# Performance work log

Measured on AMD Instinct MI355X. Metric: run time of the kernel, lower is better.

The kernel has to match this reference:

```python
import jax, jax.numpy as jnp
import numpy as np

CODEBOOK_SIZE = 4096
CODE_DIM = 256
N = 65536
COMMITMENT_COST = 0.25


def setup_inputs() -> dict:
    key = jax.random.key(0)
    k1, k2 = jax.random.split(key)
    z_flat = jax.random.normal(k1, (N, CODE_DIM), dtype=jnp.float32)
    # embedding initialized uniform(-1/codebook_size, 1/codebook_size) as in torch module
    emb_weight = jax.random.uniform(
        k2, (CODEBOOK_SIZE, CODE_DIM), dtype=jnp.float32,
        minval=-1.0 / CODEBOOK_SIZE, maxval=1.0 / CODEBOOK_SIZE)
    return {"z_flat": z_flat, "emb_weight": emb_weight}


def reference(z_flat, emb_weight):
    # squared L2 distances: [N, K] = |z|^2 + |e|^2 - 2 z e^T
    distances = (
        jnp.sum(z_flat ** 2, axis=1, keepdims=True)
        + jnp.sum(emb_weight ** 2, axis=1)
        - 2.0 * jnp.matmul(z_flat, emb_weight.T)
    )
    indices = jnp.argmin(distances, axis=1)  # [N]
    quantized = emb_weight[indices]          # [N, code_dim]

    e_latent_loss = jnp.mean((jax.lax.stop_gradient(quantized) - z_flat) ** 2)
    q_latent_loss = jnp.mean((quantized - jax.lax.stop_gradient(z_flat)) ** 2)
    loss = q_latent_loss + COMMITMENT_COST * e_latent_loss

    # straight-through estimator
    quantized_st = z_flat + jax.lax.stop_gradient(quantized - z_flat)
    return (loss, quantized_st, indices)
```

## Files before the change

kernel.cpp:

```cpp
#include <hip/hip_runtime.h>

#define KCODES 4096
#define DIM    256
#define NROWS  65536
#define MARGIN 4.0e-4f
#define DSLACK 3.0e-5f
#define LCAP   4096
#define CPAD   32
#define LSTRIDE (DIM + 4)

typedef unsigned long long u64;
typedef unsigned int  uint;
typedef unsigned short ushort;
typedef __attribute__((ext_vector_type(8))) short bf16x8;
typedef __attribute__((ext_vector_type(4))) float f32x4;

typedef __attribute__((address_space(3))) uint lds_u32_t;
typedef __attribute__((address_space(1))) uint glb_u32_t;

__device__ __forceinline__ void g2lds16(const void* g, void* l) {
    __builtin_amdgcn_global_load_lds((const glb_u32_t*)g, (lds_u32_t*)l, 16, 0, 0);
}

__device__ __forceinline__ float dppmin_quad(float m) {
    m = fminf(m, __int_as_float(__builtin_amdgcn_update_dpp(0, __float_as_int(m), 0xB1, 0xF, 0xF, true)));
    m = fminf(m, __int_as_float(__builtin_amdgcn_update_dpp(0, __float_as_int(m), 0x4E, 0xF, 0xF, true)));
    return m;
}
__device__ __forceinline__ float dppmin_row16(float m) {
    m = fminf(m, __int_as_float(__builtin_amdgcn_update_dpp(0, __float_as_int(m), 0x124, 0xF, 0xF, true)));
    m = fminf(m, __int_as_float(__builtin_amdgcn_update_dpp(0, __float_as_int(m), 0x128, 0xF, 0xF, true)));
    return m;
}
__device__ __forceinline__ uint dppor_row16(uint v) {
    v |= (uint)__builtin_amdgcn_update_dpp(0, (int)v, 0x124, 0xF, 0xF, true);
    v |= (uint)__builtin_amdgcn_update_dpp(0, (int)v, 0x128, 0xF, 0xF, true);
    return v;
}


__device__ __forceinline__ float np_half_sum128(const float4* __restrict__ p4) {
    #pragma clang fp contract(off)
    float4 v0 = p4[0], v1 = p4[1];
    float r0 = v0.x * v0.x, r1 = v0.y * v0.y, r2 = v0.z * v0.z, r3 = v0.w * v0.w;
    float r4 = v1.x * v1.x, r5 = v1.y * v1.y, r6 = v1.z * v1.z, r7 = v1.w * v1.w;
    #pragma unroll
    for (int i = 1; i < 16; ++i) {
        float4 a = p4[2 * i], b = p4[2 * i + 1];
        r0 += a.x * a.x; r1 += a.y * a.y; r2 += a.z * a.z; r3 += a.w * a.w;
        r4 += b.x * b.x; r5 += b.y * b.y; r6 += b.z * b.z; r7 += b.w * b.w;
    }
    return ((r0 + r1) + (r2 + r3)) + ((r4 + r5) + (r6 + r7));
}

__global__ void k_rownorm(const float* __restrict__ src, float* __restrict__ dst, int nrows) {
    int r = blockIdx.x * blockDim.x + threadIdx.x;
    if (r >= nrows) return;
    const float4* p4 = (const float4*)(src + (size_t)r * DIM);
    float s;
    {
        #pragma clang fp contract(off)
        s = np_half_sum128(p4) + np_half_sum128(p4 + 32);
    }
    dst[r] = s;
}

__device__ __forceinline__ float f32_dist(float Cr, float ebc, double accv) {
    #pragma clang fp contract(off)
    float A = Cr + ebc;
    float B = 2.0f * (float)accv;
    return A - B;
}

__device__ __forceinline__ ushort f2bf(float f) {
    uint u = __float_as_uint(f);
    return (ushort)((u + 0x7fffu + ((u >> 16) & 1u)) >> 16);
}


__global__ void k_split(const float* __restrict__ src, ushort* __restrict__ dst, int n8) {
    int i = blockIdx.x * blockDim.x + threadIdx.x;
    if (i >= n8) return;
    const float4* s4 = (const float4*)src;
    float4 a = s4[2 * i], b = s4[2 * i + 1];
    uint4 ov;
    ov.x = (uint)f2bf(a.x) | ((uint)f2bf(a.y) << 16);
    ov.y = (uint)f2bf(a.z) | ((uint)f2bf(a.w) << 16);
    ov.z = (uint)f2bf(b.x) | ((uint)f2bf(b.y) << 16);
    ov.w = (uint)f2bf(b.z) | ((uint)f2bf(b.w) << 16);
    *(uint4*)&dst[8 * i] = ov;
}

__global__ void k_init(int* __restrict__ cnt) {
    cnt[blockIdx.x * 256 + threadIdx.x] = 0;
}

__global__ __launch_bounds__(256, 2)
void k_gemm(const ushort* __restrict__ zh, const ushort* __restrict__ eh,
            const float* __restrict__ Crow, const float* __restrict__ eb2,
            float* __restrict__ tk, uint* __restrict__ tk2) {
    __shared__ __align__(16) ushort Bs[2][64 * 256];

    const int t = threadIdx.x;
    const int lane = t & 63;
    const int w = t >> 6;
    const int l15 = lane & 15, l4 = lane >> 4;
    const int row0w = blockIdx.x * 128 + w * 32;

    const char* ebp = (const char*)eh;

    auto stage = [&](int buf, int ct2) {
        const char* base = ebp + (size_t)ct2 * 64 * 512;
        #pragma unroll
        for (int i = 0; i < 8; ++i) {
            int idx = i * 256 + t;
            int code = idx >> 5;
            int c16  = idx & 31;
            int src  = (code << 9) + ((c16 ^ (code & 7)) << 4);
            g2lds16(base + src, (char*)Bs[buf] + idx * 16);
        }
    };

    bf16x8 a[2][8];
    #pragma unroll
    for (int f = 0; f < 2; ++f)
        #pragma unroll
        for (int ks = 0; ks < 8; ++ks)
            a[f][ks] = *(const bf16x8*)&zh[(size_t)(row0w + f * 16 + l15) * 256 + ks * 32 + l4 * 8];

    float crf[8];
    #pragma unroll
    for (int f = 0; f < 2; ++f)
        #pragma unroll
        for (int rg = 0; rg < 4; ++rg)
            crf[f * 4 + rg] = Crow[row0w + f * 16 + l4 * 4 + rg];

    float mprev[8];

    stage(0, 0);
    __syncthreads();

    #pragma unroll 2
    for (int ct2 = 0; ct2 < 64; ++ct2) {
        int buf = ct2 & 1;
        if (ct2 < 63) stage(buf ^ 1, ct2 + 1);

        f32x4 acc[2][4];
        #pragma unroll
        for (int f = 0; f < 2; ++f)
            #pragma unroll
            for (int cg = 0; cg < 4; ++cg) acc[f][cg] = (f32x4){0.f, 0.f, 0.f, 0.f};

        const ushort* Bb = Bs[buf];
        #pragma unroll
        for (int ks = 0; ks < 8; ++ks) {
            bf16x8 bfv[4];
            #pragma unroll
            for (int cg = 0; cg < 4; ++cg) {
                int rB = cg * 16 + l15;
                int off = rB * 256 + ((ks * 32 + l4 * 8) ^ ((l15 & 7) << 3));
                bfv[cg] = *(const bf16x8*)&Bb[off];
            }
            #pragma unroll
            for (int f = 0; f < 2; ++f)
                #pragma unroll
                for (int cg = 0; cg < 4; ++cg)
                    acc[f][cg] = __builtin_amdgcn_mfma_f32_16x16x32_bf16(
                        a[f][ks], bfv[cg], acc[f][cg], 0, 0, 0);
        }

        float ebv[4];
        #pragma unroll
        for (int cg = 0; cg < 4; ++cg) ebv[cg] = eb2[ct2 * 64 + cg * 16 + l15];

        #pragma unroll
        for (int f = 0; f < 2; ++f) {
            #pragma unroll
            for (int rg = 0; rg < 4; ++rg) {
                float m;
                {
                    #pragma clang fp contract(off)
                    m = 1e38f;
                    #pragma unroll
                    for (int cg = 0; cg < 4; ++cg) {
                        float A = crf[f * 4 + rg] + ebv[cg];
                        float d = A - 2.0f * acc[f][cg][rg];
                        m = fminf(m, d);
                    }
                }
                m = dppmin_quad(m);
                if ((ct2 & 1) == 0) {
                    mprev[f * 4 + rg] = m;
                } else {
                    m = fminf(m, mprev[f * 4 + rg]);
                    float mt = dppmin_row16(m);
                    int q = (int)((m - mt) * 1e5f);
                    q = q > 255 ? 255 : q;
                    uint pk = (uint)q << (8 * (l15 >> 2));
                    pk = dppor_row16(pk);
                    if (l15 == 0) {
                        int grow = row0w + f * 16 + l4 * 4 + rg;
                        int tt = ct2 >> 1;
                        tk [(size_t)tt * NROWS + grow] = mt;
                        tk2[(size_t)tt * NROWS + grow] = pk;
                    }
                }
            }
        }
        __syncthreads();
    }
}

__global__ void k_lists(const float* __restrict__ tk, const uint* __restrict__ tk2,
                        int* __restrict__ cnt, int* __restrict__ list,
                        u64* __restrict__ fkey) {
    int row = blockIdx.x * 256 + threadIdx.x;
    int lane = threadIdx.x & 63;
    float tm[32]; uint pk[32];
    #pragma unroll
    for (int tt = 0; tt < 32; ++tt) {
        tm[tt] = tk [(size_t)tt * NROWS + row];
        pk[tt] = tk2[(size_t)tt * NROWS + row];
    }
    float best = tm[0];
    #pragma unroll
    for (int tt = 1; tt < 32; ++tt) best = fminf(best, tm[tt]);
    fkey[row] = ~0ull;
    float cutoff = best + (MARGIN + DSLACK);

    #pragma unroll
    for (int tt = 0; tt < 32; ++tt) {
        #pragma unroll
        for (int p = 0; p < 4; ++p) {
            float v = tm[tt] + (float)((pk[tt] >> (8 * p)) & 255u) * 1e-5f;
            bool pred = v <= cutoff;
            u64 mask = __ballot(pred);
            if (mask) {
                int sub = tt * 4 + p;
                int nq = __popcll(mask);
                int rank = __popcll(mask & ((1ull << lane) - 1ull));
                int base = 0;
                if (lane == 0) base = atomicAdd(&cnt[sub * CPAD], nq);
                base = __shfl(base, 0, 64);
                int pos = base + rank;
                if (pred && pos < LCAP) list[sub * LCAP + pos] = row;
            }
        }
    }
}

__global__ __launch_bounds__(256, 2)
void k_exact(const float* __restrict__ z, const float* __restrict__ e,
             const float* __restrict__ Crow, const float* __restrict__ eb2,
             const int* __restrict__ list, const int* __restrict__ cnt,
             u64* __restrict__ fkey) {
    __shared__ __align__(16) float ex[32][260];
    __shared__ __align__(16) float zx[32][260];
    __shared__ int rows[32];
    __shared__ u64 keytab[32][17];
    const int sub = blockIdx.x;
    const int tile = sub >> 2, qq = sub & 3;
    const int nct = cnt[sub * CPAD];
    const int t = threadIdx.x;
    const int rp = t & 15, cs = t >> 4;

    {
        int cc = t >> 3, c8 = t & 7;
        int gcode = tile * 128 + (cc >> 2) * 16 + qq * 4 + (cc & 3);
        const float4* src = (const float4*)(e + (size_t)gcode * DIM);
        float4* dr = (float4*)ex[cc];
        #pragma unroll
        for (int j = 0; j < 8; ++j) dr[c8 + 8 * j] = src[c8 + 8 * j];
    }
    const int gc0 = tile * 128 + (cs >> 2) * 16 + qq * 4 + (cs & 3);
    const int gc1 = tile * 128 + ((cs >> 2) + 4) * 16 + qq * 4 + (cs & 3);
    const float ebc0 = eb2[gc0];
    const float ebc1 = eb2[gc1];

    for (int base = blockIdx.y * 32; base < nct; base += gridDim.y * 32) {
        __syncthreads();
        if (t < 32) {
            int i = base + t;
            rows[t] = list[sub * LCAP + (i < nct ? i : nct - 1)];
        }
        __syncthreads();
        {
            int rr = t >> 3, c8 = t & 7;
            const float4* src = (const float4*)(z + (size_t)rows[rr] * DIM);
            float4* dr = (float4*)zx[rr];
            #pragma unroll
            for (int j = 0; j < 8; ++j) dr[c8 + 8 * j] = src[c8 + 8 * j];
        }
        __syncthreads();

        double a00 = 0.0, a01 = 0.0, a10 = 0.0, a11 = 0.0;
        const float4* z0 = (const float4*)zx[rp];
        const float4* z1 = (const float4*)zx[rp + 16];
        const float4* e0 = (const float4*)ex[cs];
        const float4* e1 = (const float4*)ex[cs + 16];
        #pragma unroll 8
        for (int d4 = 0; d4 < 64; ++d4) {
            float4 x0 = z0[d4], x1 = z1[d4], y0 = e0[d4], y1 = e1[d4];
            a00 += (double)x0.x * (double)y0.x; a00 += (double)x0.y * (double)y0.y;
            a00 += (double)x0.z * (double)y0.z; a00 += (double)x0.w * (double)y0.w;
            a01 += (double)x0.x * (double)y1.x; a01 += (double)x0.y * (double)y1.y;
            a01 += (double)x0.z * (double)y1.z; a01 += (double)x0.w * (double)y1.w;
            a10 += (double)x1.x * (double)y0.x; a10 += (double)x1.y * (double)y0.y;
            a10 += (double)x1.z * (double)y0.z; a10 += (double)x1.w * (double)y0.w;
            a11 += (double)x1.x * (double)y1.x; a11 += (double)x1.y * (double)y1.y;
            a11 += (double)x1.z * (double)y1.z; a11 += (double)x1.w * (double)y1.w;
        }
        int r0 = rows[rp], r1 = rows[rp + 16];
        float C0 = Crow[r0], C1 = Crow[r1];
        u64 k00 = ((u64)__float_as_uint(f32_dist(C0, ebc0, a00)) << 32) | (u64)gc0;
        u64 k01 = ((u64)__float_as_uint(f32_dist(C0, ebc1, a01)) << 32) | (u64)gc1;
        u64 k10 = ((u64)__float_as_uint(f32_dist(C1, ebc0, a10)) << 32) | (u64)gc0;
        u64 k11 = ((u64)__float_as_uint(f32_dist(C1, ebc1, a11)) << 32) | (u64)gc1;
        keytab[rp][cs]      = k00 < k01 ? k00 : k01;
        keytab[rp + 16][cs] = k10 < k11 ? k10 : k11;
        __syncthreads();
        if (t < 32) {
            u64 kb = keytab[t][0];
            #pragma unroll
            for (int j = 1; j < 16; ++j) {
                u64 k = keytab[t][j];
                kb = k < kb ? k : kb;
            }
            atomicMin((unsigned long long*)&fkey[rows[t]], kb);
        }
    }
}

__global__ __launch_bounds__(256)
void k_gather(const float* __restrict__ z, const float* __restrict__ e,
              const u64* __restrict__ fkey, float* __restrict__ out,
              double* __restrict__ partial) {
    __shared__ double lred[4];
    const int t = threadIdx.x;
    const int row = blockIdx.x * 32 + (t >> 3);
    const int c8 = t & 7;
    const int idx = (int)(fkey[row] & 0xffffffffull);
    if (c8 == 0) out[1 + (size_t)NROWS * DIM + row] = (float)idx;
    const float4* zr = (const float4*)(z + (size_t)row * DIM);
    const float4* er = (const float4*)(e + (size_t)idx * DIM);
    float4* orow = (float4*)(out + 1 + (size_t)row * DIM);
    double lacc = 0.0;
    #pragma unroll
    for (int j = 0; j < 8; ++j) {
        float4 q = er[c8 + 8 * j];
        float4 zv = zr[c8 + 8 * j];
        orow[c8 + 8 * j] = q;
        double d0 = (double)q.x - (double)zv.x;
        double d1 = (double)q.y - (double)zv.y;
        double d2 = (double)q.z - (double)zv.z;
        double d3 = (double)q.w - (double)zv.w;
        lacc += d0 * d0 + d1 * d1 + d2 * d2 + d3 * d3;
    }
    for (int off = 32; off > 0; off >>= 1) lacc += __shfl_down(lacc, off, 64);
    if ((t & 63) == 0) lred[t >> 6] = lacc;
    __syncthreads();
    if (t == 0) partial[blockIdx.x] = lred[0] + lred[1] + lred[2] + lred[3];
}

__global__ void k_finish(const double* __restrict__ partial, float* __restrict__ out, int n) {
    __shared__ double s[256];
    double a = 0.0;
    for (int i = threadIdx.x; i < n; i += 256) a += partial[i];
    s[threadIdx.x] = a;
    __syncthreads();
    for (int off = 128; off > 0; off >>= 1) {
        if (threadIdx.x < off) s[threadIdx.x] += s[threadIdx.x + off];
        __syncthreads();
    }
    if (threadIdx.x == 0)
        out[0] = (float)(1.25 * s[0] / ((double)NROWS * (double)DIM));
}


__global__ __launch_bounds__(256, 1)
void k_main_slow(const float* __restrict__ z, const float* __restrict__ e,
                 const float* __restrict__ Crow, const float* __restrict__ eb2,
                 float* __restrict__ out, double* __restrict__ partial) {
    __shared__ float  zt[64][LSTRIDE];
    __shared__ float  et[64][LSTRIDE];
    __shared__ float  redd[64][17];
    __shared__ int    redi[64][17];
    __shared__ int    bsel[64];
    __shared__ double lred[4];

    const int t  = threadIdx.x;
    const int tx = t & 15;
    const int ty = t >> 4;
    const int row0 = blockIdx.x * 64;

    {
        const float4* zsrc = (const float4*)(z + (size_t)row0 * DIM);
        for (int i = t; i < 64 * (DIM / 4); i += 256) {
            int r = i >> 6, c4 = i & 63;
            *(float4*)&zt[r][c4 * 4] = zsrc[r * (DIM / 4) + c4];
        }
    }
    float Cr[4];
    #pragma unroll
    for (int ri = 0; ri < 4; ++ri) Cr[ri] = Crow[row0 + ty * 4 + ri];
    float bestd[4]; int besti[4];
    #pragma unroll
    for (int ri = 0; ri < 4; ++ri) { bestd[ri] = __int_as_float(0x7f800000); besti[ri] = 0; }

    for (int kt = 0; kt < KCODES / 64; ++kt) {
        __syncthreads();
        {
            const float4* esrc = (const float4*)(e + (size_t)kt * 64 * DIM);
            for (int i = t; i < 64 * (DIM / 4); i += 256) {
                int r = i >> 6, c4 = i & 63;
                *(float4*)&et[r][c4 * 4] = esrc[r * (DIM / 4) + c4];
            }
        }
        __syncthreads();
        double acc[4][4];
        #pragma unroll
        for (int a = 0; a < 4; ++a)
            #pragma unroll
            for (int b = 0; b < 4; ++b) acc[a][b] = 0.0;
        #pragma unroll 4
        for (int d4 = 0; d4 < DIM / 4; ++d4) {
            float4 za[4], ea[4];
            #pragma unroll
            for (int ri = 0; ri < 4; ++ri) za[ri] = *(const float4*)&zt[ty * 4 + ri][d4 * 4];
            #pragma unroll
            for (int ci = 0; ci < 4; ++ci) ea[ci] = *(const float4*)&et[tx + 16 * ci][d4 * 4];
            #pragma unroll
            for (int ri = 0; ri < 4; ++ri)
                #pragma unroll
                for (int ci = 0; ci < 4; ++ci)
                    acc[ri][ci] += (double)za[ri].x * (double)ea[ci].x
                                 + (double)za[ri].y * (double)ea[ci].y
                                 + (double)za[ri].z * (double)ea[ci].z
                                 + (double)za[ri].w * (double)ea[ci].w;
        }
        #pragma unroll
        for (int ci = 0; ci < 4; ++ci) {
            int c = kt * 64 + tx + 16 * ci;
            float ebc = eb2[c];
            #pragma unroll
            for (int ri = 0; ri < 4; ++ri) {
                float d = f32_dist(Cr[ri], ebc, acc[ri][ci]);
                if (d < bestd[ri]) { bestd[ri] = d; besti[ri] = c; }
            }
        }
    }
    __syncthreads();
    #pragma unroll
    for (int ri = 0; ri < 4; ++ri) {
        redd[ty * 4 + ri][tx] = bestd[ri];
        redi[ty * 4 + ri][tx] = besti[ri];
    }
    __syncthreads();
    if (t < 64) {
        float bd = redd[t][0]; int bi = redi[t][0];
        for (int j = 1; j < 16; ++j) {
            float d = redd[t][j]; int i2 = redi[t][j];
            if (d < bd || (d == bd && i2 < bi)) { bd = d; bi = i2; }
        }
        bsel[t] = bi;
        out[1 + (size_t)NROWS * DIM + row0 + t] = (float)bi;
    }
    __syncthreads();
    double lacc = 0.0;
    {
        int r = t >> 2, qd = (t & 3) * 64;
        int bi = bsel[r];
        const float* qrow = e + (size_t)bi * DIM + qd;
        float* orow = out + 1 + (size_t)(row0 + r) * DIM + qd;
        #pragma unroll 4
        for (int d = 0; d < 64; ++d) {
            float qv = qrow[d], zv = zt[r][qd + d];
            double df = (double)qv - (double)zv;
            lacc += df * df;
            orow[d] = qv;
        }
    }
    for (int off = 32; off > 0; off >>= 1) lacc += __shfl_down(lacc, off, 64);
    if ((t & 63) == 0) lred[t >> 6] = lacc;
    __syncthreads();
    if (t == 0) partial[blockIdx.x] = lred[0] + lred[1] + lred[2] + lred[3];
}


extern "C" void kernel_launch(void* const* d_in, const int* in_sizes, int n_in,
                              void* d_out, int out_size, void* d_ws, size_t ws_size,
                              hipStream_t stream) {
    const float* z = (const float*)d_in[0];
    const float* e = (const float*)d_in[1];
    float* out = (float*)d_out;
    char* w = (char*)d_ws;

    size_t o = 0;
    auto take = [&](size_t b) { size_t r = o; o = (o + b + 255) & ~(size_t)255; return r; };
    size_t o_zh = take((size_t)NROWS * DIM * 2);
    size_t o_eh = take((size_t)KCODES * DIM * 2);
    size_t o_cr = take((size_t)NROWS * 4);
    size_t o_eb = take((size_t)KCODES * 4);
    size_t o_tk = take((size_t)32 * NROWS * 4);
    size_t o_t2 = take((size_t)32 * NROWS * 4);
    size_t o_fk = take((size_t)NROWS * 8);
    size_t o_cn = take((size_t)128 * CPAD * 4);
    size_t o_ls = take((size_t)128 * LCAP * 4);
    size_t o_pt = take((size_t)2048 * 8);
    size_t need = o;

    if (ws_size >= need) {
        ushort* zh = (ushort*)(w + o_zh);
        ushort* eh = (ushort*)(w + o_eh);
        float* Cr  = (float*)(w + o_cr);
        float* eb  = (float*)(w + o_eb);
        float* tk  = (float*)(w + o_tk);
        uint*  tk2 = (uint*)(w + o_t2);
        u64*   fk  = (u64*)(w + o_fk);
        int*   cn  = (int*)(w + o_cn);
        int*   ls  = (int*)(w + o_ls);
        double* pt = (double*)(w + o_pt);

        k_split<<<NROWS * DIM / 8 / 256, 256, 0, stream>>>(z, zh, NROWS * DIM / 8);
        k_split<<<KCODES * DIM / 8 / 256, 256, 0, stream>>>(e, eh, KCODES * DIM / 8);
        k_rownorm<<<NROWS / 256, 256, 0, stream>>>(z, Cr, NROWS);
        k_rownorm<<<KCODES / 256, 256, 0, stream>>>(e, eb, KCODES);
        k_init<<<(128 * CPAD) / 256, 256, 0, stream>>>(cn);
        k_gemm<<<NROWS / 128, 256, 0, stream>>>(zh, eh, Cr, eb, tk, tk2);
        k_lists<<<NROWS / 256, 256, 0, stream>>>(tk, tk2, cn, ls, fk);
        dim3 ge(128, 16);
        k_exact<<<ge, 256, 0, stream>>>(z, e, Cr, eb, ls, cn, fk);
        k_gather<<<NROWS / 32, 256, 0, stream>>>(z, e, fk, out, pt);
        k_finish<<<1, 256, 0, stream>>>(pt, out, 2048);
    } else {
        float* Cr  = (float*)w;
        float* eb  = Cr + NROWS;
        double* pt = (double*)(eb + KCODES);
        k_rownorm<<<NROWS / 256, 256, 0, stream>>>(z, Cr, NROWS);
        k_rownorm<<<KCODES / 256, 256, 0, stream>>>(e, eb, KCODES);
        k_main_slow<<<NROWS / 64, 256, 0, stream>>>(z, e, Cr, eb, out, pt);
        k_finish<<<1, 256, 0, stream>>>(pt, out, NROWS / 64);
    }
}
```

Before: 344.7 us.

## Software-pipeline distance epilogue with next tile's MFMA loop using dual accumulators

```diff
diff --git a/kernel.cpp b/kernel.cpp
--- a/kernel.cpp
+++ b/kernel.cpp
@@ -136,22 +136,11 @@
             crf[f * 4 + rg] = Crow[row0w + f * 16 + l4 * 4 + rg];
 
     float mprev[8];
-
-    stage(0, 0);
-    __syncthreads();
-
-    #pragma unroll 2
-    for (int ct2 = 0; ct2 < 64; ++ct2) {
-        int buf = ct2 & 1;
-        if (ct2 < 63) stage(buf ^ 1, ct2 + 1);
-
-        f32x4 acc[2][4];
-        #pragma unroll
-        for (int f = 0; f < 2; ++f)
-            #pragma unroll
-            for (int cg = 0; cg < 4; ++cg) acc[f][cg] = (f32x4){0.f, 0.f, 0.f, 0.f};
-
-        const ushort* Bb = Bs[buf];
+    const f32x4 fzero = (f32x4){0.f, 0.f, 0.f, 0.f};
+    f32x4 accA[2][4], accB[2][4];
+    float ebvA[4], ebvB[4];
+
+    auto ksloop = [&](const ushort* Bb, f32x4 (&acc)[2][4]) {
         #pragma unroll
         for (int ks = 0; ks < 8; ++ks) {
             bf16x8 bfv[4];
@@ -161,35 +150,28 @@
                 int off = rB * 256 + ((ks * 32 + l4 * 8) ^ ((l15 & 7) << 3));
                 bfv[cg] = *(const bf16x8*)&Bb[off];
             }
+            __builtin_amdgcn_s_setprio(1);
             #pragma unroll
             for (int f = 0; f < 2; ++f)
                 #pragma unroll
                 for (int cg = 0; cg < 4; ++cg)
                     acc[f][cg] = __builtin_amdgcn_mfma_f32_16x16x32_bf16(
-                        a[f][ks], bfv[cg], acc[f][cg], 0, 0, 0);
-        }
-
-        float ebv[4];
-        #pragma unroll
-        for (int cg = 0; cg < 4; ++cg) ebv[cg] = eb2[ct2 * 64 + cg * 16 + l15];
-
+                        a[f][ks], bfv[cg], ks == 0 ? fzero : acc[f][cg], 0, 0, 0);
+            __builtin_amdgcn_s_setprio(0);
+        }
+    };
+
+    auto epi = [&](f32x4 (&acc)[2][4], const float (&ebv)[4], int ct2, bool odd) {
         #pragma unroll
         for (int f = 0; f < 2; ++f) {
             #pragma unroll
             for (int rg = 0; rg < 4; ++rg) {
-                float m;
-                {
-                    #pragma clang fp contract(off)
-                    m = 1e38f;
-                    #pragma unroll
-                    for (int cg = 0; cg < 4; ++cg) {
-                        float A = crf[f * 4 + rg] + ebv[cg];
-                        float d = A - 2.0f * acc[f][cg][rg];
-                        m = fminf(m, d);
-                    }
-                }
+                float m =    fmaf(-2.0f, acc[f][0][rg], ebv[0]);
+                m = fminf(m, fmaf(-2.0f, acc[f][1][rg], ebv[1]));
+                m = fminf(m, fmaf(-2.0f, acc[f][2][rg], ebv[2]));
+                m = fminf(m, fmaf(-2.0f, acc[f][3][rg], ebv[3]));
                 m = dppmin_quad(m);
-                if ((ct2 & 1) == 0) {
+                if (!odd) {
                     mprev[f * 4 + rg] = m;
                 } else {
                     m = fminf(m, mprev[f * 4 + rg]);
@@ -201,14 +183,38 @@
                     if (l15 == 0) {
                         int grow = row0w + f * 16 + l4 * 4 + rg;
                         int tt = ct2 >> 1;
-                        tk [(size_t)tt * NROWS + grow] = mt;
+                        tk [(size_t)tt * NROWS + grow] = crf[f * 4 + rg] + mt;
                         tk2[(size_t)tt * NROWS + grow] = pk;
                     }
                 }
             }
         }
-        __syncthreads();
-    }
+    };
+
+    stage(0, 0);
+    #pragma unroll
+    for (int cg = 0; cg < 4; ++cg) ebvA[cg] = eb2[cg * 16 + l15];
+    __syncthreads();
+
+    for (int tp = 0; tp < 32; ++tp) {
+        int t0 = 2 * tp;
+        stage(1, t0 + 1);
+        if (tp > 0) epi(accB, ebvB, t0 - 1, true);
+        ksloop(Bs[0], accA);
+        __syncthreads();
+
+        if (tp < 31) stage(0, t0 + 2);
+        #pragma unroll
+        for (int cg = 0; cg < 4; ++cg) ebvB[cg] = eb2[(t0 + 1) * 64 + cg * 16 + l15];
+        epi(accA, ebvA, t0, false);
+        if (tp < 31) {
+            #pragma unroll
+            for (int cg = 0; cg < 4; ++cg) ebvA[cg] = eb2[(t0 + 2) * 64 + cg * 16 + l15];
+        }
+        ksloop(Bs[1], accB);
+        __syncthreads();
+    }
+    epi(accB, ebvB, 63, true);
 }
 
 __global__ void k_lists(const float* __restrict__ tk, const uint* __restrict__ tk2,
```

Result: faster. 330.0 us (-4.3%).
